# Kernel optimization log

Hardware: AMD Instinct MI355X
Metric: run time of the kernel (lower is better)

Reference implementation:

```python
import jax, jax.numpy as jnp
import numpy as np
from jax import lax

B, CIN, COUT, K, H, W = 16, 256, 256, 3, 128, 128
R = 16  # LoRA rank


def setup_inputs() -> dict:
    key = jax.random.key(0)
    ks = jax.random.split(key, 16)
    s = 0.05
    return {
        "x": jax.random.normal(ks[0], (B, CIN, H, W), jnp.float32),
        "wms": jax.random.normal(ks[1], (2, B, 32), jnp.float32),
        "conv_w": jax.random.normal(ks[2], (COUT, CIN, K, K), jnp.float32) * s,
        "conv_b": jax.random.normal(ks[3], (COUT,), jnp.float32) * s,
        "e1_w1": jax.random.normal(ks[4], (128, 32), jnp.float32) * s,
        "e1_b1": jax.random.normal(ks[5], (128,), jnp.float32) * s,
        "e1_w2": jax.random.normal(ks[6], (256, 128), jnp.float32) * s,
        "e1_b2": jax.random.normal(ks[7], (256,), jnp.float32) * s,
        "e2_w1": jax.random.normal(ks[8], (128, 32), jnp.float32) * s,
        "e2_b1": jax.random.normal(ks[9], (128,), jnp.float32) * s,
        "e2_w2": jax.random.normal(ks[10], (256, 128), jnp.float32) * s,
        "e2_b2": jax.random.normal(ks[11], (256,), jnp.float32) * s,
        "lora_A1": jax.random.normal(ks[12], (R, CIN * K), jnp.float32),
        "lora_A2": jax.random.normal(ks[13], (R, CIN * K), jnp.float32),
        "lora_B": jax.random.normal(ks[14], (COUT * K, R), jnp.float32) * s,
    }


def _embed(v, w1, b1, w2, b2):
    # Linear(32,128) -> LeakyReLU(0.2) -> Linear(128,256)
    h = v @ w1.T + b1
    h = jnp.where(h >= 0, h, 0.2 * h)
    return h @ w2.T + b2


def _conv_same(x, w):
    # NCHW conv, stride 1, padding 1
    return lax.conv_general_dilated(x, w, (1, 1), [(1, 1), (1, 1)],
                                    dimension_numbers=("NCHW", "OIHW", "NCHW"))


def reference(x, wms, conv_w, conv_b, e1_w1, e1_b1, e1_w2, e1_b2,
              e2_w1, e2_b1, e2_w2, e2_b2, lora_A1, lora_A2, lora_B):
    wm1, wm2 = wms[0], wms[1]
    coff1 = _embed(wm1, e1_w1, e1_b1, e1_w2, e1_b2).reshape(B, R, R)
    coff2 = _embed(wm2, e2_w1, e2_b1, e2_w2, e2_b2).reshape(B, R, R)

    org = _conv_same(x, conv_w) + conv_b[None, :, None, None]

    # per-sample LoRA weights: (COUT*K, R) @ (R,R) @ (R, CIN*K) -> (B, COUT, CIN, K, K)
    wA = jnp.einsum('pr,brq,qc->bpc', lora_B, coff1, lora_A1).reshape(B, COUT, CIN, K, K)
    wB = jnp.einsum('pr,brq,qc->bpc', lora_B, coff2, lora_A2).reshape(B, COUT, CIN, K, K)

    def per_sample_conv(xi, wi):
        return _conv_same(xi[None], wi)[0]

    outA = jax.vmap(per_sample_conv)(x, wA)
    outB = jax.vmap(per_sample_conv)(x, wB)
    return org + outA + outB
```

## Files before the change

### kernel.cpp

```cpp
#include <hip/hip_runtime.h>
#include <hip/hip_bf16.h>
#include <stdint.h>

typedef __bf16 bf16x8 __attribute__((ext_vector_type(8)));
typedef float f32x4 __attribute__((ext_vector_type(4)));
typedef unsigned short ushort8v __attribute__((ext_vector_type(8)));

#define NB    16
#define CIN   256
#define COUT  256
#define HH    128
#define WW    128

#define OFF_ZROW  0u
#define OFF_COFF  (1u << 16)
#define OFF_TMPS  (1u << 17)
#define OFF_WEFF  (1u << 20)
#define OFF_XT    (20u * 1024u * 1024u)
#define XT_PER_B  (128u * 128u * 256u * 2u)

__device__ inline void gload16(const void* g, void* l) {
  __builtin_amdgcn_global_load_lds(
      (const __attribute__((address_space(1))) void*)g,
      (__attribute__((address_space(3))) void*)l, 16, 0, 0);
}

__device__ inline ushort f2bf(float f) {
  __hip_bfloat16 h = __float2bfloat16(f);
  union { __hip_bfloat16 b; ushort u; } cv;
  cv.b = h;
  return cv.u;
}

__global__ void k_coff(const float* __restrict__ wms,
                       const float* __restrict__ w1a, const float* __restrict__ b1a,
                       const float* __restrict__ w2a, const float* __restrict__ b2a,
                       const float* __restrict__ w1b, const float* __restrict__ b1b,
                       const float* __restrict__ w2b, const float* __restrict__ b2b,
                       float* __restrict__ coff) {
  int br = blockIdx.x >> 4, b = blockIdx.x & 15;
  const float* w1 = br ? w1b : w1a;
  const float* b1 = br ? b1b : b1a;
  const float* w2 = br ? w2b : w2a;
  const float* b2 = br ? b2b : b2a;
  const float* v = wms + (br * 16 + b) * 32;
  __shared__ float h[128];
  int t = threadIdx.x;
  if (t < 128) {
    float a = b1[t];
#pragma unroll
    for (int i = 0; i < 32; ++i) a += w1[t * 32 + i] * v[i];
    h[t] = a >= 0.f ? a : 0.2f * a;
  }
  __syncthreads();
  float a = b2[t];
  for (int j = 0; j < 128; ++j) a += w2[t * 128 + j] * h[j];
  coff[(br * 16 + b) * 256 + t] = a;
}

__global__ void k_tmps(const float* __restrict__ coff,
                       const float* __restrict__ A1, const float* __restrict__ A2,
                       float* __restrict__ tmpS) {
  int b = blockIdx.x >> 4, r = blockIdx.x & 15;
  __shared__ float c1[16], c2[16];
  int t = threadIdx.x;
  if (t < 16) {
    c1[t] = coff[b * 256 + r * 16 + t];
    c2[t] = coff[(16 + b) * 256 + r * 16 + t];
  }
  __syncthreads();
  for (int c = t; c < 768; c += 256) {
    float s = 0.f;
#pragma unroll
    for (int q = 0; q < 16; ++q) s += c1[q] * A1[q * 768 + c] + c2[q] * A2[q * 768 + c];
    tmpS[(b * 16 + r) * 768 + c] = s;
  }
}

__global__ __launch_bounds__(256) void k_prep(
    const float* __restrict__ conv_w, const float* __restrict__ loraB,
    const float* __restrict__ tmpS, __hip_bfloat16* __restrict__ Weff,
    const float* __restrict__ x, __hip_bfloat16* __restrict__ xT,
    int b0, int nweff) {
  __shared__ ushort sbuf[32 * 132];
  int bid = blockIdx.x;
  int tid = threadIdx.x;

  if (bid < nweff) {
    int co = bid & 255, b = bid >> 8;
    ushort* obuf = sbuf;
    float* Bs = (float*)(sbuf + 2304);
    if (tid < 48) Bs[(tid >> 4) * 16 + (tid & 15)] =
        loraB[(co * 3 + (tid >> 4)) * 16 + (tid & 15)];
    __syncthreads();
    const float* T = tmpS + (size_t)b * 16 * 768;
    const float* W = conv_w + (size_t)co * 2304;
#pragma unroll
    for (int k = 0; k < 3; ++k) {
#pragma unroll
      for (int cc = 0; cc < 3; ++cc) {
        int c = cc * 256 + tid;
        float s = W[k * 768 + c];
        const float* Bk = Bs + k * 16;
#pragma unroll
        for (int r = 0; r < 16; ++r) s += Bk[r] * T[r * 768 + c];
        int f = k * 768 + c;
        int ci = f / 9, tt = f - ci * 9;
        obuf[tt * 256 + ci] = f2bf(s);
      }
    }
    __syncthreads();
#pragma unroll
    for (int tt = 0; tt < 9; ++tt)
      ((ushort*)Weff)[((size_t)(b * 9 + tt) * 256 + co) * 256 + tid] =
          obuf[tt * 256 + tid];
  } else {
    int xbid = bid - nweff;
    int cb = xbid & 7, h = (xbid >> 3) & 127, bp = xbid >> 10;
    int b = b0 + bp;
    ushort(*t)[132] = (ushort(*)[132])sbuf;
    int ci2 = tid >> 5, w4 = (tid & 31) * 4;
    const float* srcb = x + ((size_t)(b * 256 + cb * 32) * 128 + h) * 128;
#pragma unroll
    for (int k = 0; k < 4; ++k) {
      int c = ci2 + k * 8;
      float4 v = *(const float4*)(srcb + (size_t)c * 16384 + w4);
      ushort4 u;
      u.x = f2bf(v.x);
      u.y = f2bf(v.y);
      u.z = f2bf(v.z);
      u.w = f2bf(v.w);
      *(ushort4*)&t[c][w4] = u;
    }
    __syncthreads();
    int w = tid >> 1, hf = tid & 1;
    ushort8v o0, o1;
#pragma unroll
    for (int j = 0; j < 8; ++j) {
      o0[j] = t[hf * 16 + j][w];
      o1[j] = t[hf * 16 + 8 + j][w];
    }
    ushort* dst = (ushort*)xT + (size_t)bp * 128 * 128 * 256 +
                  ((size_t)h * 128 + w) * 256 + cb * 32 + hf * 16;
    *(ushort8v*)dst = o0;
    *(ushort8v*)(dst + 8) = o1;
  }
}

__global__ __launch_bounds__(256, 2) void k_conv(
    const __hip_bfloat16* __restrict__ xT,
    const __hip_bfloat16* __restrict__ Weff,
    const __hip_bfloat16* __restrict__ zrow,
    const float* __restrict__ cbias,
    float* __restrict__ out, int b0) {
  __shared__ __align__(16) __hip_bfloat16 xs[4 * 130 * 32];
  __shared__ __align__(16) __hip_bfloat16 wbuf[3 * 128 * 32];

  int nwg = gridDim.x;
  int bid0 = blockIdx.x;
  int bid = (bid0 & 7) * (nwg >> 3) + (bid0 >> 3);

  int hp = bid & 63, coh = (bid >> 6) & 1, bp = bid >> 7;
  int b = b0 + bp;
  int h0 = hp * 2;

  int tid = threadIdx.x;
  int wid = tid >> 6, lane = tid & 63;
  int l15 = lane & 15, lh = lane >> 4;
  int row = wid >> 1;
  int w0 = (wid & 1) * 64;
  int lrow = lane >> 2;
  int sgx = (lane & 3) ^ (((1 + lrow) >> 1) & 3);
  int sgw = (lane & 3) ^ ((lrow >> 1) & 3);
  int asw = (l15 >> 1) & 3;

  if (tid < 256) {
    int ri = tid >> 6, which = (tid >> 5) & 1, ci = tid & 31;
    ((ushort*)xs)[ri * 4160 + (which ? 129 : 0) * 32 + ci] = 0;
  }

  int a_base = l15 * 32 + (lh ^ asw) * 8;
  int b_base0 = (w0 + l15 + 0) * 32 + ((lh ^ (((l15 + 0) >> 1) & 3)) * 8);
  int b_base1 = (w0 + l15 + 1) * 32 + ((lh ^ (((l15 + 1) >> 1) & 3)) * 8);
  int b_base2 = (w0 + l15 + 2) * 32 + ((lh ^ (((l15 + 2) >> 1) & 3)) * 8);
  int xoff = lrow * 256 + sgx * 8;
  int woff = (coh * 128 + lrow) * 256 + sgw * 8;

  const __hip_bfloat16* xTb = xT + (size_t)bp * 128 * 128 * 256;
  const __hip_bfloat16* r0 = (h0 > 0)   ? xTb + (size_t)(h0 - 1) * 32768 : zrow;
  const __hip_bfloat16* r1 = xTb + (size_t)h0 * 32768;
  const __hip_bfloat16* r2 = xTb + (size_t)(h0 + 1) * 32768;
  const __hip_bfloat16* r3 = (h0 < 126) ? xTb + (size_t)(h0 + 2) * 32768 : zrow;

  f32x4 acc[8][4];
#pragma unroll
  for (int mf = 0; mf < 8; ++mf)
#pragma unroll
    for (int nf = 0; nf < 4; ++nf) acc[mf][nf] = (f32x4){0.f, 0.f, 0.f, 0.f};

  for (int cb8 = 0; cb8 < 8; ++cb8) {
    int c0 = cb8 * 32;
    __syncthreads();

#pragma unroll
    for (int k = 0; k < 8; ++k) {
      const int ri = k >> 1;
      int wblk = (k & 1) * 4 + wid;
      const __hip_bfloat16* rp = (ri == 0) ? r0 : ((ri == 1) ? r1 : ((ri == 2) ? r2 : r3));
      gload16((const void*)(rp + wblk * 4096 + c0 + xoff),
              (void*)(xs + ri * 4160 + (1 + wblk * 16) * 32));
    }

#pragma unroll 1
    for (int kh = 0; kh < 3; ++kh) {
      if (kh) __syncthreads();
      const __hip_bfloat16* wtap =
          Weff + ((size_t)(b * 9 + kh * 3) << 16) + c0 + woff;
#pragma unroll
      for (int k = 0; k < 6; ++k) {
        const int kw = k >> 1;
        int cblk = (k & 1) * 4 + wid;
        gload16((const void*)(wtap + kw * 65536 + cblk * 4096),
                (void*)(wbuf + kw * 4096 + cblk * 512));
      }
      __syncthreads();

#pragma unroll
      for (int kw = 0; kw < 3; ++kw) {
        int bb = (kw == 0) ? b_base0 : ((kw == 1) ? b_base1 : b_base2);
        bf16x8 af[8], bfr[4];
#pragma unroll
        for (int mf = 0; mf < 8; ++mf)
          af[mf] = *(const bf16x8*)&wbuf[kw * 4096 + a_base + mf * 512];
#pragma unroll
        for (int nf = 0; nf < 4; ++nf)
          bfr[nf] = *(const bf16x8*)&xs[(row + kh) * 4160 + bb + nf * 512];
#pragma unroll
        for (int mf = 0; mf < 8; ++mf)
#pragma unroll
          for (int nf = 0; nf < 4; ++nf)
            acc[mf][nf] = __builtin_amdgcn_mfma_f32_16x16x32_bf16(af[mf], bfr[nf],
                                                                  acc[mf][nf], 0, 0, 0);
      }
    }
  }

#pragma unroll
  for (int mf = 0; mf < 8; ++mf) {
    int cobase = coh * 128 + mf * 16 + lh * 4;
#pragma unroll
    for (int r = 0; r < 4; ++r) {
      int co = cobase + r;
      float bias = cbias[co];
      size_t obase = ((size_t)(b * 256 + co) * 128 + (h0 + row)) * 128 + w0 + l15;
#pragma unroll
      for (int nf = 0; nf < 4; ++nf) out[obase + nf * 16] = acc[mf][nf][r] + bias;
    }
  }
}

extern "C" void kernel_launch(void* const* d_in, const int* in_sizes, int n_in,
                              void* d_out, int out_size, void* d_ws, size_t ws_size,
                              hipStream_t stream) {
  const float* x      = (const float*)d_in[0];
  const float* wms    = (const float*)d_in[1];
  const float* conv_w = (const float*)d_in[2];
  const float* conv_b = (const float*)d_in[3];
  const float* e1w1   = (const float*)d_in[4];
  const float* e1b1   = (const float*)d_in[5];
  const float* e1w2   = (const float*)d_in[6];
  const float* e1b2   = (const float*)d_in[7];
  const float* e2w1   = (const float*)d_in[8];
  const float* e2b1   = (const float*)d_in[9];
  const float* e2w2   = (const float*)d_in[10];
  const float* e2b2   = (const float*)d_in[11];
  const float* A1     = (const float*)d_in[12];
  const float* A2     = (const float*)d_in[13];
  const float* loraB  = (const float*)d_in[14];
  float* out = (float*)d_out;

  uint8_t* ws = (uint8_t*)d_ws;
  __hip_bfloat16* zrow = (__hip_bfloat16*)(ws + OFF_ZROW);
  float* coff          = (float*)(ws + OFF_COFF);
  float* tmpS          = (float*)(ws + OFF_TMPS);
  __hip_bfloat16* Weff = (__hip_bfloat16*)(ws + OFF_WEFF);
  __hip_bfloat16* xT   = (__hip_bfloat16*)(ws + OFF_XT);

  int G = 16;
  while (G > 1 && (size_t)OFF_XT + (size_t)G * XT_PER_B > ws_size) G >>= 1;

  hipMemsetAsync(zrow, 0, 65536, stream);
  k_coff<<<32, 256, 0, stream>>>(wms, e1w1, e1b1, e1w2, e1b2, e2w1, e2b1, e2w2, e2b2, coff);
  k_tmps<<<256, 256, 0, stream>>>(coff, A1, A2, tmpS);
  for (int g = 0; g < 16; g += G) {
    int nweff = (g == 0) ? 16 * 256 : 0;
    k_prep<<<nweff + G * 1024, 256, 0, stream>>>(conv_w, loraB, tmpS, Weff,
                                                 x, xT, g, nweff);
    k_conv<<<G * 128, 256, 0, stream>>>(xT, Weff, zrow, conv_b, out, g);
  }
}
```

Before: 414.9 us.

## Overlap x transpose of second half-batch with convolution of first half

The per-sample conv and the x-to-bf16 NHWC transpose are restructured so that one mixed kernel runs conv blocks for batches 0-7 alongside transpose blocks for batches 8-15. A final conv kernel then handles the second half. Separate prep and conv phases were serialized before, so this lets the memory-bound transpose hide behind the MFMA-bound conv. The cost is a kernel with mixed block types sharing one LDS allocation, plus an extra launch.

```diff
diff --git a/kernel.cpp b/kernel.cpp
--- a/kernel.cpp
+++ b/kernel.cpp
@@ -18,6 +18,8 @@
 #define OFF_WEFF  (1u << 20)
 #define OFF_XT    (20u * 1024u * 1024u)
 #define XT_PER_B  (128u * 128u * 256u * 2u)
+
+#define CONV_LDS_BYTES (4 * 130 * 32 * 2 + 3 * 128 * 32 * 2)
 
 __device__ inline void gload16(const void* g, void* l) {
   __builtin_amdgcn_global_load_lds(
@@ -77,87 +79,81 @@
   }
 }
 
-__global__ __launch_bounds__(256) void k_prep(
-    const float* __restrict__ conv_w, const float* __restrict__ loraB,
-    const float* __restrict__ tmpS, __hip_bfloat16* __restrict__ Weff,
-    const float* __restrict__ x, __hip_bfloat16* __restrict__ xT,
-    int b0, int nweff) {
-  __shared__ ushort sbuf[32 * 132];
-  int bid = blockIdx.x;
+
+__device__ __forceinline__ void weff_block(
+    int bid, ushort* sbuf, const float* __restrict__ conv_w,
+    const float* __restrict__ loraB, const float* __restrict__ tmpS,
+    __hip_bfloat16* __restrict__ Weff) {
+  int co = bid & 255, b = bid >> 8;
   int tid = threadIdx.x;
-
-  if (bid < nweff) {
-    int co = bid & 255, b = bid >> 8;
-    ushort* obuf = sbuf;
-    float* Bs = (float*)(sbuf + 2304);
-    if (tid < 48) Bs[(tid >> 4) * 16 + (tid & 15)] =
-        loraB[(co * 3 + (tid >> 4)) * 16 + (tid & 15)];
-    __syncthreads();
-    const float* T = tmpS + (size_t)b * 16 * 768;
-    const float* W = conv_w + (size_t)co * 2304;
-#pragma unroll
-    for (int k = 0; k < 3; ++k) {
-#pragma unroll
-      for (int cc = 0; cc < 3; ++cc) {
-        int c = cc * 256 + tid;
-        float s = W[k * 768 + c];
-        const float* Bk = Bs + k * 16;
-#pragma unroll
-        for (int r = 0; r < 16; ++r) s += Bk[r] * T[r * 768 + c];
-        int f = k * 768 + c;
-        int ci = f / 9, tt = f - ci * 9;
-        obuf[tt * 256 + ci] = f2bf(s);
-      }
-    }
-    __syncthreads();
-#pragma unroll
-    for (int tt = 0; tt < 9; ++tt)
-      ((ushort*)Weff)[((size_t)(b * 9 + tt) * 256 + co) * 256 + tid] =
-          obuf[tt * 256 + tid];
-  } else {
-    int xbid = bid - nweff;
-    int cb = xbid & 7, h = (xbid >> 3) & 127, bp = xbid >> 10;
-    int b = b0 + bp;
-    ushort(*t)[132] = (ushort(*)[132])sbuf;
-    int ci2 = tid >> 5, w4 = (tid & 31) * 4;
-    const float* srcb = x + ((size_t)(b * 256 + cb * 32) * 128 + h) * 128;
-#pragma unroll
-    for (int k = 0; k < 4; ++k) {
-      int c = ci2 + k * 8;
-      float4 v = *(const float4*)(srcb + (size_t)c * 16384 + w4);
-      ushort4 u;
-      u.x = f2bf(v.x);
-      u.y = f2bf(v.y);
-      u.z = f2bf(v.z);
-      u.w = f2bf(v.w);
-      *(ushort4*)&t[c][w4] = u;
-    }
-    __syncthreads();
-    int w = tid >> 1, hf = tid & 1;
-    ushort8v o0, o1;
-#pragma unroll
-    for (int j = 0; j < 8; ++j) {
-      o0[j] = t[hf * 16 + j][w];
-      o1[j] = t[hf * 16 + 8 + j][w];
-    }
-    ushort* dst = (ushort*)xT + (size_t)bp * 128 * 128 * 256 +
-                  ((size_t)h * 128 + w) * 256 + cb * 32 + hf * 16;
-    *(ushort8v*)dst = o0;
-    *(ushort8v*)(dst + 8) = o1;
-  }
-}
-
-__global__ __launch_bounds__(256, 2) void k_conv(
+  ushort* obuf = sbuf;
+  float* Bs = (float*)(sbuf + 2304);
+  if (tid < 48)
+    Bs[(tid >> 4) * 16 + (tid & 15)] = loraB[(co * 3 + (tid >> 4)) * 16 + (tid & 15)];
+  __syncthreads();
+  const float* T = tmpS + (size_t)b * 16 * 768;
+  const float* W = conv_w + (size_t)co * 2304;
+#pragma unroll
+  for (int k = 0; k < 3; ++k) {
+#pragma unroll
+    for (int cc = 0; cc < 3; ++cc) {
+      int c = cc * 256 + tid;
+      float s = W[k * 768 + c];
+      const float* Bk = Bs + k * 16;
+#pragma unroll
+      for (int r = 0; r < 16; ++r) s += Bk[r] * T[r * 768 + c];
+      int f = k * 768 + c;
+      int ci = f / 9, tt = f - ci * 9;
+      obuf[tt * 256 + ci] = f2bf(s);
+    }
+  }
+  __syncthreads();
+#pragma unroll
+  for (int tt = 0; tt < 9; ++tt)
+    ((ushort*)Weff)[((size_t)(b * 9 + tt) * 256 + co) * 256 + tid] = obuf[tt * 256 + tid];
+}
+
+__device__ __forceinline__ void xt_block(
+    int xbid, int b0, int xslot0, ushort* sbuf,
+    const float* __restrict__ x, __hip_bfloat16* __restrict__ xT) {
+  int cb = xbid & 7, h = (xbid >> 3) & 127, bp = xbid >> 10;
+  int b = b0 + bp;
+  int tid = threadIdx.x;
+  ushort(*t)[132] = (ushort(*)[132])sbuf;
+  int ci2 = tid >> 5, w4 = (tid & 31) * 4;
+  const float* srcb = x + ((size_t)(b * 256 + cb * 32) * 128 + h) * 128;
+#pragma unroll
+  for (int k = 0; k < 4; ++k) {
+    int c = ci2 + k * 8;
+    float4 v = *(const float4*)(srcb + (size_t)c * 16384 + w4);
+    ushort4 u;
+    u.x = f2bf(v.x);
+    u.y = f2bf(v.y);
+    u.z = f2bf(v.z);
+    u.w = f2bf(v.w);
+    *(ushort4*)&t[c][w4] = u;
+  }
+  __syncthreads();
+  int w = tid >> 1, hf = tid & 1;
+  ushort8v o0, o1;
+#pragma unroll
+  for (int j = 0; j < 8; ++j) {
+    o0[j] = t[hf * 16 + j][w];
+    o1[j] = t[hf * 16 + 8 + j][w];
+  }
+  ushort* dst = (ushort*)xT + (size_t)(xslot0 + bp) * 128 * 128 * 256 +
+                ((size_t)h * 128 + w) * 256 + cb * 32 + hf * 16;
+  *(ushort8v*)dst = o0;
+  *(ushort8v*)(dst + 8) = o1;
+}
+
+__device__ __forceinline__ void conv_block(
+    int bid0, int nwg, int b0, int xslot0,
+    __hip_bfloat16* xs, __hip_bfloat16* wbuf,
     const __hip_bfloat16* __restrict__ xT,
     const __hip_bfloat16* __restrict__ Weff,
     const __hip_bfloat16* __restrict__ zrow,
-    const float* __restrict__ cbias,
-    float* __restrict__ out, int b0) {
-  __shared__ __align__(16) __hip_bfloat16 xs[4 * 130 * 32];
-  __shared__ __align__(16) __hip_bfloat16 wbuf[3 * 128 * 32];
-
-  int nwg = gridDim.x;
-  int bid0 = blockIdx.x;
+    const float* __restrict__ cbias, float* __restrict__ out) {
   int bid = (bid0 & 7) * (nwg >> 3) + (bid0 >> 3);
 
   int hp = bid & 63, coh = (bid >> 6) & 1, bp = bid >> 7;
@@ -174,7 +170,7 @@
   int sgw = (lane & 3) ^ ((lrow >> 1) & 3);
   int asw = (l15 >> 1) & 3;
 
-  if (tid < 256) {
+  {
     int ri = tid >> 6, which = (tid >> 5) & 1, ci = tid & 31;
     ((ushort*)xs)[ri * 4160 + (which ? 129 : 0) * 32 + ci] = 0;
   }
@@ -186,7 +182,7 @@
   int xoff = lrow * 256 + sgx * 8;
   int woff = (coh * 128 + lrow) * 256 + sgw * 8;
 
-  const __hip_bfloat16* xTb = xT + (size_t)bp * 128 * 128 * 256;
+  const __hip_bfloat16* xTb = xT + (size_t)(xslot0 + bp) * 128 * 128 * 256;
   const __hip_bfloat16* r0 = (h0 > 0)   ? xTb + (size_t)(h0 - 1) * 32768 : zrow;
   const __hip_bfloat16* r1 = xTb + (size_t)h0 * 32768;
   const __hip_bfloat16* r2 = xTb + (size_t)(h0 + 1) * 32768;
@@ -257,6 +253,46 @@
       for (int nf = 0; nf < 4; ++nf) out[obase + nf * 16] = acc[mf][nf][r] + bias;
     }
   }
+}
+
+
+__global__ __launch_bounds__(256) void k_prep(
+    const float* __restrict__ conv_w, const float* __restrict__ loraB,
+    const float* __restrict__ tmpS, __hip_bfloat16* __restrict__ Weff,
+    const float* __restrict__ x, __hip_bfloat16* __restrict__ xT,
+    int b0, int xslot0, int nweff) {
+  __shared__ __align__(16) ushort sbuf[32 * 132];
+  int bid = blockIdx.x;
+  if (bid < nweff)
+    weff_block(bid, sbuf, conv_w, loraB, tmpS, Weff);
+  else
+    xt_block(bid - nweff, b0, xslot0, sbuf, x, xT);
+}
+
+__global__ __launch_bounds__(256, 2) void k_mix(
+    const __hip_bfloat16* __restrict__ xT_c, __hip_bfloat16* __restrict__ xT_w,
+    const __hip_bfloat16* __restrict__ Weff,
+    const __hip_bfloat16* __restrict__ zrow, const float* __restrict__ cbias,
+    float* __restrict__ out, const float* __restrict__ x,
+    int nconv, int b0c, int xs0c, int b0x, int xs0x) {
+  __shared__ __align__(16) char smem[CONV_LDS_BYTES];
+  int bid = blockIdx.x;
+  if (bid < nconv)
+    conv_block(bid, nconv, b0c, xs0c, (__hip_bfloat16*)smem,
+               (__hip_bfloat16*)(smem + 33280), xT_c, Weff, zrow, cbias, out);
+  else
+    xt_block(bid - nconv, b0x, xs0x, (ushort*)smem, x, xT_w);
+}
+
+__global__ __launch_bounds__(256, 2) void k_conv(
+    const __hip_bfloat16* __restrict__ xT,
+    const __hip_bfloat16* __restrict__ Weff,
+    const __hip_bfloat16* __restrict__ zrow,
+    const float* __restrict__ cbias, float* __restrict__ out,
+    int b0, int xslot0) {
+  __shared__ __align__(16) char smem[CONV_LDS_BYTES];
+  conv_block(blockIdx.x, gridDim.x, b0, xslot0, (__hip_bfloat16*)smem,
+             (__hip_bfloat16*)(smem + 33280), xT, Weff, zrow, cbias, out);
 }
 
 extern "C" void kernel_launch(void* const* d_in, const int* in_sizes, int n_in,
@@ -292,10 +328,19 @@
   hipMemsetAsync(zrow, 0, 65536, stream);
   k_coff<<<32, 256, 0, stream>>>(wms, e1w1, e1b1, e1w2, e1b2, e2w1, e2b1, e2w2, e2b2, coff);
   k_tmps<<<256, 256, 0, stream>>>(coff, A1, A2, tmpS);
-  for (int g = 0; g < 16; g += G) {
-    int nweff = (g == 0) ? 16 * 256 : 0;
-    k_prep<<<nweff + G * 1024, 256, 0, stream>>>(conv_w, loraB, tmpS, Weff,
-                                                 x, xT, g, nweff);
-    k_conv<<<G * 128, 256, 0, stream>>>(xT, Weff, zrow, conv_b, out, g);
-  }
-}
+
+  if (G == 16) {
+    k_prep<<<4096 + 8 * 1024, 256, 0, stream>>>(conv_w, loraB, tmpS, Weff,
+                                                x, xT, 0, 0, 4096);
+    k_mix<<<8 * 128 + 8 * 1024, 256, 0, stream>>>(xT, xT, Weff, zrow, conv_b,
+                                                  out, x, 8 * 128, 0, 0, 8, 8);
+    k_conv<<<8 * 128, 256, 0, stream>>>(xT, Weff, zrow, conv_b, out, 8, 8);
+  } else {
+    for (int g = 0; g < 16; g += G) {
+      int nweff = (g == 0) ? 4096 : 0;
+      k_prep<<<nweff + G * 1024, 256, 0, stream>>>(conv_w, loraB, tmpS, Weff,
+                                                   x, xT, g, 0, nweff);
+      k_conv<<<G * 128, 256, 0, stream>>>(xT, Weff, zrow, conv_b, out, g, 0);
+    }
+  }
+}
```

After: 406.4 us. 1.02x faster.
